# Performance work log

Hardware: AMD Instinct MI355X
Metric: run time of the kernel (lower is better)

## Reference

```python
import jax, jax.numpy as jnp
import numpy as np

B, S, MW = 128, 256, 21          # batch, sentence length, max word length
VOCAB, E_CHAR, E_WORD, K = 100, 50, 256, 5


def setup_inputs() -> dict:
    key = jax.random.key(0)
    ks = jax.random.split(key, 6)
    padded_sents = jax.random.randint(ks[0], (B, S, MW), 0, VOCAB)
    emb_table = jax.random.normal(ks[1], (VOCAB, E_CHAR), jnp.float32) * 0.1
    emb_table = emb_table.at[0].set(0.0)  # pad_token_idx row zeroed (padding_idx)
    conv_w = jax.random.normal(ks[2], (E_WORD, E_CHAR, K), jnp.float32) * 0.05
    conv_b = jnp.zeros((E_WORD,), jnp.float32)
    w_proj = jax.random.normal(ks[3], (E_WORD, E_WORD), jnp.float32) * 0.05
    b_proj = jnp.zeros((E_WORD,), jnp.float32)
    w_gate = jax.random.normal(ks[4], (E_WORD, E_WORD), jnp.float32) * 0.05
    b_gate = jnp.zeros((E_WORD,), jnp.float32)
    return {
        "padded_sents": padded_sents,
        "emb_table": emb_table,
        "conv_w": conv_w,
        "conv_b": conv_b,
        "w_proj": w_proj,
        "b_proj": b_proj,
        "w_gate": w_gate,
        "b_gate": b_gate,
    }


def reference(padded_sents, emb_table, conv_w, conv_b, w_proj, b_proj, w_gate, b_gate):
    b, s, mw = padded_sents.shape
    # char embedding lookup: [B,S,MW,E_CHAR]
    x = emb_table[padded_sents]
    # fold (B,S) into one batch dim and move channels first: [B*S, E_CHAR, MW]
    x = x.reshape(b * s, mw, -1).transpose(0, 2, 1)
    # Conv1d VALID over char positions: [B*S, E_WORD, MW-K+1]
    y = jax.lax.conv_general_dilated(
        x, conv_w, window_strides=(1,), padding="VALID",
        dimension_numbers=("NCH", "OIH", "NCH"))
    y = jax.nn.relu(y + conv_b[None, :, None])
    # max-pool over remaining char positions: [B*S, E_WORD]
    y = jnp.max(y, axis=2)
    # Highway network
    proj = jax.nn.relu(y @ w_proj.T + b_proj)
    gate = jax.nn.sigmoid(y @ w_gate.T + b_gate)
    out = gate * proj + (1.0 - gate) * y
    # dropout in eval mode (identity)
    return out.reshape(b, s, -1)
```

## Files before the change

### kernel.cpp

```cpp
#include <hip/hip_runtime.h>

#define B_     128
#define S_     256
#define MW_    21
#define VOCAB_ 100
#define EC_    50
#define EW_    256
#define KW_    5
#define T_     17
#define NW_    (B_ * S_)
#define GROWS  (VOCAB_ * KW_)
#define WPB    128

typedef _Float16 f16x8 __attribute__((ext_vector_type(8)));
typedef float    f32x4 __attribute__((ext_vector_type(4)));

__global__ __launch_bounds__(256) void k_prep(const float* __restrict__ emb,
                                              const float* __restrict__ cw,
                                              const float* __restrict__ Wp,
                                              const float* __restrict__ Wg,
                                              _Float16* __restrict__ g,
                                              _Float16* __restrict__ wpf,
                                              _Float16* __restrict__ wgf) {
  const int bi = blockIdx.x;
  if (bi < GROWS) {
    __shared__ float es[EC_];
    const int v = bi / KW_;
    const int k = bi % KW_;
    const int o = threadIdx.x;
    if (threadIdx.x < EC_) es[threadIdx.x] = emb[v * EC_ + threadIdx.x];
    __syncthreads();
    float acc = 0.f;
#pragma unroll
    for (int i = 0; i < EC_; ++i)
      acc += es[i] * cw[(o * EC_ + i) * KW_ + k];
    g[bi * EW_ + o] = (_Float16)acc;
  } else {
    const int fl  = (bi - GROWS) * 256 + threadIdx.x;
    const int nt  = fl >> 9;
    const int rem = fl & 511;
    const int ks  = rem >> 6;
    const int l   = rem & 63;
    const int n   = nt * 16 + (l & 15);
    const int kc  = ks * 32 + (l >> 4) * 8;
    const int src = n * EW_ + kc;
    const float4 p0 = *(const float4*)&Wp[src], p1 = *(const float4*)&Wp[src + 4];
    const float4 q0 = *(const float4*)&Wg[src], q1 = *(const float4*)&Wg[src + 4];
    f16x8 hp = {(_Float16)p0.x, (_Float16)p0.y, (_Float16)p0.z, (_Float16)p0.w,
                (_Float16)p1.x, (_Float16)p1.y, (_Float16)p1.z, (_Float16)p1.w};
    f16x8 hg = {(_Float16)q0.x, (_Float16)q0.y, (_Float16)q0.z, (_Float16)q0.w,
                (_Float16)q1.x, (_Float16)q1.y, (_Float16)q1.z, (_Float16)q1.w};
    *(f16x8*)&wpf[fl * 8] = hp;
    *(f16x8*)&wgf[fl * 8] = hg;
  }
}

__global__ __launch_bounds__(512, 2) void k_mega(const int* __restrict__ idx,
                                                 const _Float16* __restrict__ g,
                                                 const float* __restrict__ cb,
                                                 const _Float16* __restrict__ wpf,
                                                 const _Float16* __restrict__ wgf,
                                                 const float* __restrict__ bp,
                                                 const float* __restrict__ bg,
                                                 float* __restrict__ out) {
  __shared__ __align__(16) _Float16 lds[32768 + GROWS * 64];
  _Float16* y_s = lds;
  _Float16* g_s = lds + 32768;

  const int tid  = threadIdx.x;
  const int wave = tid >> 6, lane = tid & 63;
  const int m0 = blockIdx.x * WPB;
  const int wq = lane >> 3, og = lane & 7;

#pragma unroll
  for (int i = 0; i < 8; ++i) {
    const int c = tid + i * 512;
    if (c < GROWS * 8) {
      const int row = c >> 3, cc = c & 7;
      *(f16x8*)&g_s[row * 64 + cc * 8] = *(const f16x8*)&g[row * EW_ + cc * 8];
    }
  }
  __syncthreads();

  f16x8 pre[8];
#pragma unroll
  for (int chunk = 0; chunk < 4; ++chunk) {
    const int oc0 = chunk * 64;
    if (chunk < 3) {
#pragma unroll
      for (int i = 0; i < 8; ++i) {
        const int c = tid + i * 512;
        if (c < GROWS * 8) {
          const int row = c >> 3, cc = c & 7;
          pre[i] = *(const f16x8*)&g[row * EW_ + oc0 + 64 + cc * 8];
        }
      }
    }

    f16x8 bias;
#pragma unroll
    for (int j = 0; j < 8; ++j) bias[j] = (_Float16)cb[oc0 + og * 8 + j];

    const int ks_w    = chunk * 2 + (og >> 2);
    const int lane_hi = (og & 3) << 4;

#pragma unroll
    for (int it = 0; it < 2; ++it) {
      const int wl = it * 64 + wave * 8 + wq;
      const int* __restrict__ ip = idx + (m0 + wl) * MW_;
      int base[MW_];
#pragma unroll
      for (int c = 0; c < MW_; ++c)
        base[c] = ip[c] * (KW_ * 64) + og * 8;

      const _Float16 NEG = (_Float16)(-60000.0f);
      f16x8 mx = {NEG, NEG, NEG, NEG, NEG, NEG, NEG, NEG};
#pragma unroll
      for (int t = 0; t < T_; ++t) {
        f16x8 s = *(const f16x8*)&g_s[base[t]];
#pragma unroll
        for (int k = 1; k < KW_; ++k)
          s += *(const f16x8*)&g_s[base[t + k] + k * 64];
        mx = __builtin_elementwise_max(mx, s);
      }
      const f16x8 zero8 = {0, 0, 0, 0, 0, 0, 0, 0};
      mx = __builtin_elementwise_max(mx + bias, zero8);

      const int mt = wl >> 4;
      const int lt = ((wl & 15) | lane_hi) ^ og;
      *(f16x8*)&y_s[((mt * 8 + ks_w) * 64 + lt) * 8] = mx;
    }
    __syncthreads();
    if (chunk < 3) {
#pragma unroll
      for (int i = 0; i < 8; ++i) {
        const int c = tid + i * 512;
        if (c < GROWS * 8) {
          const int row = c >> 3, cc = c & 7;
          *(f16x8*)&g_s[row * 64 + cc * 8] = pre[i];
        }
      }
      __syncthreads();
    }
  }

  const int mtp = wave >> 1, nh = wave & 1;
  const int quad = lane >> 4, r16 = lane & 15;

  f16x8 a[2][8];
#pragma unroll
  for (int mi = 0; mi < 2; ++mi)
#pragma unroll
    for (int ks = 0; ks < 8; ++ks) {
      const int key = ((ks & 1) << 2) | quad;
      a[mi][ks] = *(const f16x8*)&y_s[(((mtp * 2 + mi) * 8 + ks) * 64 + (lane ^ key)) * 8];
    }

  const f32x4 zero = {0.f, 0.f, 0.f, 0.f};
#pragma unroll
  for (int h = 0; h < 2; ++h) {
    f32x4 accp[2][4], accg[2][4];
#pragma unroll
    for (int mi = 0; mi < 2; ++mi)
#pragma unroll
      for (int nf = 0; nf < 4; ++nf) { accp[mi][nf] = zero; accg[mi][nf] = zero; }

#pragma unroll
    for (int nf = 0; nf < 4; ++nf) {
      const int nt = h * 8 + nh * 4 + nf;
#pragma unroll
      for (int ks = 0; ks < 8; ++ks) {
        const int off = ((nt * 8 + ks) * 64 + lane) * 8;
        const f16x8 bpv = *(const f16x8*)&wpf[off];
        const f16x8 bgv = *(const f16x8*)&wgf[off];
#pragma unroll
        for (int mi = 0; mi < 2; ++mi) {
          accp[mi][nf] = __builtin_amdgcn_mfma_f32_16x16x32_f16(a[mi][ks], bpv, accp[mi][nf], 0, 0, 0);
          accg[mi][nf] = __builtin_amdgcn_mfma_f32_16x16x32_f16(a[mi][ks], bgv, accg[mi][nf], 0, 0, 0);
        }
      }
    }

#pragma unroll
    for (int mi = 0; mi < 2; ++mi) {
      const int mt = mtp * 2 + mi;
#pragma unroll
      for (int nf = 0; nf < 4; ++nf) {
        const int n = h * 128 + nh * 64 + nf * 16 + r16;
        const float bpn = bp[n];
        const float bgn = bg[n];
        const int ks_e = n >> 5;
        const int lane_e = ((n >> 3) & 3) << 4;
        const int og_e = (n >> 3) & 7;
        const int je = n & 7;
#pragma unroll
        for (int reg = 0; reg < 4; ++reg) {
          const int m = mt * 16 + quad * 4 + reg;
          float p = fmaxf(accp[mi][nf][reg] + bpn, 0.f);
          const float gz = accg[mi][nf][reg] + bgn;
          const float gate = 1.f / (1.f + __expf(-gz));
          const float yv =
              (float)y_s[((mt * 8 + ks_e) * 64 + (((m & 15) | lane_e) ^ og_e)) * 8 + je];
          out[(m0 + m) * EW_ + n] = gate * p + (1.f - gate) * yv;
        }
      }
    }
  }
}

extern "C" void kernel_launch(void* const* d_in, const int* in_sizes, int n_in,
                              void* d_out, int out_size, void* d_ws, size_t ws_size,
                              hipStream_t stream) {
  (void)in_sizes; (void)n_in; (void)out_size; (void)ws_size;
  const int*   idx = (const int*)d_in[0];
  const float* emb = (const float*)d_in[1];
  const float* cw  = (const float*)d_in[2];
  const float* cb  = (const float*)d_in[3];
  const float* wp  = (const float*)d_in[4];
  const float* bpp = (const float*)d_in[5];
  const float* wgt = (const float*)d_in[6];
  const float* bgg = (const float*)d_in[7];
  float* out = (float*)d_out;
  _Float16* g_ws = (_Float16*)d_ws;
  _Float16* wp_f = g_ws + GROWS * EW_;
  _Float16* wg_f = wp_f + EW_ * EW_;

  k_prep<<<GROWS + 32, 256, 0, stream>>>(emb, cw, wp, wgt, g_ws, wp_f, wg_f);
  k_mega<<<NW_ / WPB, 512, 0, stream>>>(idx, g_ws, cb, wp_f, wg_f, bpp, bgg, out);
}
```

Baseline: 125.2 us.

## Stage conv weights in LDS for prep and XOR-swizzle gathered table in main kernel

The prep kernel now loads a 64-output slice of the conv weights into shared memory once per block and computes two vocab entries across all five taps per block. This replaces 500 blocks that each re-read strided global conv weights. The main kernel also XOR-swizzles the 8-element column slots of the char-conv lookup table in LDS by vocab id. This spreads the random gather reads across banks to reduce LDS bank conflicts, at the cost of a little extra index arithmetic.

```diff
diff --git a/kernel.cpp b/kernel.cpp
--- a/kernel.cpp
+++ b/kernel.cpp
@@ -11,6 +11,7 @@
 #define NW_    (B_ * S_)
 #define GROWS  (VOCAB_ * KW_)
 #define WPB    128
+#define P1B    200
 
 typedef _Float16 f16x8 __attribute__((ext_vector_type(8)));
 typedef float    f32x4 __attribute__((ext_vector_type(4)));
@@ -23,20 +24,37 @@
                                               _Float16* __restrict__ wpf,
                                               _Float16* __restrict__ wgf) {
   const int bi = blockIdx.x;
-  if (bi < GROWS) {
-    __shared__ float es[EC_];
-    const int v = bi / KW_;
-    const int k = bi % KW_;
-    const int o = threadIdx.x;
-    if (threadIdx.x < EC_) es[threadIdx.x] = emb[v * EC_ + threadIdx.x];
+  if (bi < P1B) {
+    __shared__ float ls[64 * 250];
+    const int vp = bi >> 2, ot = bi & 3;
+    const int o0 = ot * 64;
+    const int tid = threadIdx.x;
+    const float4* __restrict__ cw4 = (const float4*)cw + ot * 4000;
+#pragma unroll 4
+    for (int idx4 = tid; idx4 < 4000; idx4 += 256)
+      *(float4*)&ls[idx4 * 4] = cw4[idx4];
     __syncthreads();
-    float acc = 0.f;
-#pragma unroll
-    for (int i = 0; i < EC_; ++i)
-      acc += es[i] * cw[(o * EC_ + i) * KW_ + k];
-    g[bi * EW_ + o] = (_Float16)acc;
+
+    const int l = tid & 63, wv = tid >> 6;
+#pragma unroll
+    for (int vv = 0; vv < 2; ++vv) {
+      const int v = vp * 2 + vv;
+      const float* __restrict__ er = emb + v * EC_;
+      float acc = 0.f;
+#pragma unroll
+      for (int i = 0; i < EC_; ++i)
+        acc += er[i] * ls[l * 250 + i * KW_ + wv];
+      g[(v * KW_ + wv) * EW_ + o0 + l] = (_Float16)acc;
+      if (wv == 0) {
+        float a4 = 0.f;
+#pragma unroll
+        for (int i = 0; i < EC_; ++i)
+          a4 += er[i] * ls[l * 250 + i * KW_ + 4];
+        g[(v * KW_ + 4) * EW_ + o0 + l] = (_Float16)a4;
+      }
+    }
   } else {
-    const int fl  = (bi - GROWS) * 256 + threadIdx.x;
+    const int fl  = (bi - P1B) * 256 + threadIdx.x;
     const int nt  = fl >> 9;
     const int rem = fl & 511;
     const int ks  = rem >> 6;
@@ -77,7 +95,8 @@
     const int c = tid + i * 512;
     if (c < GROWS * 8) {
       const int row = c >> 3, cc = c & 7;
-      *(f16x8*)&g_s[row * 64 + cc * 8] = *(const f16x8*)&g[row * EW_ + cc * 8];
+      const int sl = cc ^ ((row / 5) & 7);
+      *(f16x8*)&g_s[row * 64 + sl * 8] = *(const f16x8*)&g[row * EW_ + cc * 8];
     }
   }
   __syncthreads();
@@ -110,8 +129,10 @@
       const int* __restrict__ ip = idx + (m0 + wl) * MW_;
       int base[MW_];
 #pragma unroll
-      for (int c = 0; c < MW_; ++c)
-        base[c] = ip[c] * (KW_ * 64) + og * 8;
+      for (int c = 0; c < MW_; ++c) {
+        const int ipc = ip[c];
+        base[c] = ipc * (KW_ * 64) + ((og ^ (ipc & 7)) << 3);
+      }
 
       const _Float16 NEG = (_Float16)(-60000.0f);
       f16x8 mx = {NEG, NEG, NEG, NEG, NEG, NEG, NEG, NEG};
@@ -137,7 +158,8 @@
         const int c = tid + i * 512;
         if (c < GROWS * 8) {
           const int row = c >> 3, cc = c & 7;
-          *(f16x8*)&g_s[row * 64 + cc * 8] = pre[i];
+          const int sl = cc ^ ((row / 5) & 7);
+          *(f16x8*)&g_s[row * 64 + sl * 8] = pre[i];
         }
       }
       __syncthreads();
@@ -225,6 +247,6 @@
   _Float16* wp_f = g_ws + GROWS * EW_;
   _Float16* wg_f = wp_f + EW_ * EW_;
 
-  k_prep<<<GROWS + 32, 256, 0, stream>>>(emb, cw, wp, wgt, g_ws, wp_f, wg_f);
+  k_prep<<<P1B + 32, 256, 0, stream>>>(emb, cw, wp, wgt, g_ws, wp_f, wg_f);
   k_mega<<<NW_ / WPB, 512, 0, stream>>>(idx, g_ws, cb, wp_f, wg_f, bpp, bgg, out);
 }
```

After: 124.5 us. About the same (-0.5%).
